# Performance work log

Hardware: AMD Instinct MI355X
Metric: run time of the kernel (lower is better)

Reference implementation:

```python
import jax, jax.numpy as jnp
import numpy as np
from jax.scipy.special import logsumexp

B, D, H, L, R, K = 4096, 784, 16, 4, 4, 8
D1 = D // 2
NBIS, NNEWT = 50, 3
LOG2PI = float(np.log(2.0 * np.pi))


def square_swish(h):
    # util.square_swish nonlinearity (swish-family; see notes)
    return h * jax.nn.sigmoid(h)


def mixture_terms(xv, logits, mu, log_s):
    # xv: [B, D1]; logits/mu/log_s: [B, D1, K]
    logw = jax.nn.log_softmax(logits, axis=-1)
    t = (xv[..., None] - mu) * jnp.exp(-log_s)
    log_cdf = logsumexp(logw + jax.nn.log_sigmoid(t), axis=-1)          # log F(x)
    log_sf = logsumexp(logw + jax.nn.log_sigmoid(-t), axis=-1)          # log (1-F(x))
    log_pdf = logsumexp(logw + jax.nn.log_sigmoid(t) + jax.nn.log_sigmoid(-t) - log_s, axis=-1)  # log F'(x)
    return log_cdf, log_sf, log_pdf


def invert_mixture_logit(y, logits, mu, log_s):
    # Solve logit(F(x)) = y for x: bisection (stop-grad) + Newton polish (differentiable).
    sl, sm, ss, sy = map(jax.lax.stop_gradient, (logits, mu, log_s, y))

    def body(_, lo_hi):
        lo, hi = lo_hi
        mid = 0.5 * (lo + hi)
        lc, lsf, _ = mixture_terms(mid, sl, sm, ss)
        f = lc - lsf - sy
        return jnp.where(f < 0, mid, lo), jnp.where(f < 0, hi, mid)

    lo = jnp.full_like(y, -100.0)
    hi = jnp.full_like(y, 100.0)
    lo, hi = jax.lax.fori_loop(0, NBIS, body, (lo, hi))
    xv = jax.lax.stop_gradient(0.5 * (lo + hi))
    for _ in range(NNEWT):
        lc, lsf, lp = mixture_terms(xv, logits, mu, log_s)
        logdet = lp - lc - lsf  # d/dx logit(F(x))
        xv = xv - (lc - lsf - y) * jnp.exp(-logdet)
    lc, lsf, lp = mixture_terms(xv, logits, mu, log_s)
    return xv, lp - lc - lsf


def conditioner(h_in, Wi, bi, W1l, b1l, W2l, b2l, Wo, bo):
    h = square_swish(h_in @ Wi + bi)
    for r in range(R):  # 4 resnet blocks, hidden_dim=16
        h = h + square_swish(h @ W1l[r] + b1l[r]) @ W2l[r] + b2l[r]
    return (h @ Wo + bo).reshape(-1, D1, 3 * K)


def flow_inverse(x, eps, W_in, b_in, W1, b1, W2, b2, W_out, b_out):
    # UnitGaussianPrior sample eps -> inverse coupling stack; log q via change of variables
    log_q = -0.5 * jnp.sum(eps * eps + LOG2PI, axis=-1)
    z = eps
    for l in reversed(range(L)):
        za, zb = z[:, :D1], z[:, D1:]
        if l % 2 == 1:
            za, zb = zb, za
        p = conditioner(jnp.concatenate([zb, x], axis=-1),
                        W_in[l], b_in[l], W1[l], b1[l], W2[l], b2[l], W_out[l], b_out[l])
        logits, mu, log_s = p[..., :K], p[..., K:2 * K], p[..., 2 * K:]
        xa, ld = invert_mixture_logit(za, logits, mu, log_s)
        log_q = log_q + jnp.sum(ld, axis=-1)
        if l % 2 == 0:
            z = jnp.concatenate([xa, zb], axis=-1)
        else:
            z = jnp.concatenate([zb, xa], axis=-1)
    return z, log_q


def setup_inputs():
    key = jax.random.key(0)
    ks = jax.random.split(key, 6)
    s_in = 1.0 / np.sqrt(D1 + D)
    s_h = 1.0 / np.sqrt(H)
    return {
        "x": jax.random.normal(ks[0], (B, D), jnp.float32),
        "eps": jax.random.normal(ks[1], (B, D), jnp.float32),
        "W_in": jax.random.normal(ks[2], (L, D1 + D, H), jnp.float32) * s_in,
        "b_in": jnp.zeros((L, H), jnp.float32),
        "W1": jax.random.normal(ks[3], (L, R, H, H), jnp.float32) * s_h,
        "b1": jnp.zeros((L, R, H), jnp.float32),
        "W2": jax.random.normal(ks[4], (L, R, H, H), jnp.float32) * s_h,
        "b2": jnp.zeros((L, R, H), jnp.float32),
        "W_out": jax.random.normal(ks[5], (L, H, D1 * 3 * K), jnp.float32) * 0.05,
        "b_out": jnp.zeros((L, D1 * 3 * K), jnp.float32),
    }


def reference(x, eps, W_in, b_in, W1, b1, W2, b2, W_out, b_out):
    return flow_inverse(x, eps, W_in, b_in, W1, b1, W2, b2, W_out, b_out)
```

## Files before the change

### kernel.cpp

```cpp
#include <hip/hip_runtime.h>
#include <math.h>

constexpr int cB   = 4096;
constexpr int cD   = 784;
constexpr int cD1  = 392;
constexpr int cH   = 16;
constexpr int cL   = 4;
constexpr int cR   = 4;
constexpr int cDIN = 1176;
constexpr int cPDIM = cD1 * 3 * 8;
#define LOG2PI_F 1.8378770664093453f
#define L2E_F    1.4426950408889634f
#define LN2_F    0.6931471805599453f
#define LN_LN2_F (-0.36651292058166432701f)

__device__ __forceinline__ float rcpf(float x)  { return __builtin_amdgcn_rcpf(x); }
__device__ __forceinline__ float exp2f_(float x){ return __builtin_amdgcn_exp2f(x); }
__device__ __forceinline__ float log2f_(float x){ return __builtin_amdgcn_logf(x); }
__device__ __forceinline__ float expn(float x)  { return exp2f_(x * L2E_F); }
__device__ __forceinline__ float logn(float x)  { return log2f_(x) * LN2_F; }

__global__ void __launch_bounds__(256) init_kernel(const float* __restrict__ eps,
                                                   float* __restrict__ logq) {
    const int wid  = threadIdx.x >> 6;
    const int lane = threadIdx.x & 63;
    const int b = blockIdx.x * 4 + wid;
    const float4* e = (const float4*)(eps + (size_t)b * cD);
    float sum = 0.f;
    for (int i = lane; i < cD / 4; i += 64) {
        float4 v = e[i];
        sum = fmaf(v.x, v.x, sum); sum = fmaf(v.y, v.y, sum);
        sum = fmaf(v.z, v.z, sum); sum = fmaf(v.w, v.w, sum);
    }
    #pragma unroll
    for (int off = 32; off; off >>= 1) sum += __shfl_xor(sum, off, 64);
    if (lane == 0) logq[b] = -0.5f * sum - 0.5f * (float)cD * LOG2PI_F;
}

__global__ void __launch_bounds__(256) mlp_kernel(
    const float* __restrict__ zbsrc, const float* __restrict__ x,
    const float* __restrict__ Win, const float* __restrict__ bin,
    const float* __restrict__ W1, const float* __restrict__ b1,
    const float* __restrict__ W2, const float* __restrict__ b2,
    float* __restrict__ hbuf)
{
    __shared__ float part[4][4][16];
    const int wid  = threadIdx.x >> 6;
    const int lane = threadIdx.x & 63;
    const int j = lane & 15;
    const int G = lane >> 4;
    const int bs = blockIdx.x * 8;
    const int sb = bs + (wid & 1) * 4;
    const int r0 = (wid >> 1) * 588;

    float acc[4][16];
    #pragma unroll
    for (int s = 0; s < 4; ++s)
        #pragma unroll
        for (int c = 0; c < 16; ++c) acc[s][c] = 0.f;

    const float* pz[4]; const float* px[4];
    #pragma unroll
    for (int s = 0; s < 4; ++s) {
        pz[s] = zbsrc + (size_t)(sb + s) * cD;
        px[s] = x + (size_t)(sb + s) * cD - cD1;
    }

    for (int i = r0 + lane; i < r0 + 588; i += 64) {
        const float4* wr = (const float4*)(Win + (size_t)i * cH);
        float4 w0 = wr[0], w1 = wr[1], w2 = wr[2], w3 = wr[3];
        float wv[16] = {w0.x,w0.y,w0.z,w0.w, w1.x,w1.y,w1.z,w1.w,
                        w2.x,w2.y,w2.z,w2.w, w3.x,w3.y,w3.z,w3.w};
        #pragma unroll
        for (int s = 0; s < 4; ++s) {
            const float* src = (i < cD1) ? pz[s] : px[s];
            float v = src[i];
            #pragma unroll
            for (int c = 0; c < 16; ++c) acc[s][c] = fmaf(v, wv[c], acc[s][c]);
        }
    }

    #pragma unroll
    for (int s = 0; s < 4; ++s) {
        #pragma unroll
        for (int c = 0; c < 8; ++c) {
            float sent = (lane & 8) ? acc[s][c] : acc[s][c + 8];
            float mine = (lane & 8) ? acc[s][c + 8] : acc[s][c];
            acc[s][c] = mine + __shfl_xor(sent, 8, 64);
        }
        #pragma unroll
        for (int c = 0; c < 4; ++c) {
            float sent = (lane & 4) ? acc[s][c] : acc[s][c + 4];
            float mine = (lane & 4) ? acc[s][c + 4] : acc[s][c];
            acc[s][c] = mine + __shfl_xor(sent, 4, 64);
        }
        #pragma unroll
        for (int c = 0; c < 2; ++c) {
            float sent = (lane & 2) ? acc[s][c] : acc[s][c + 2];
            float mine = (lane & 2) ? acc[s][c + 2] : acc[s][c];
            acc[s][c] = mine + __shfl_xor(sent, 2, 64);
        }
        {
            float sent = (lane & 1) ? acc[s][0] : acc[s][1];
            float mine = (lane & 1) ? acc[s][1] : acc[s][0];
            acc[s][0] = mine + __shfl_xor(sent, 1, 64);
        }
    }
    const int g4 = (lane >> 4) & 1, g5 = (lane >> 5) & 1;
    float a01, a23, colsum;
    {
        float sent = g4 ? acc[0][0] : acc[1][0];
        float keep = g4 ? acc[1][0] : acc[0][0];
        a01 = keep + __shfl_xor(sent, 16, 64);
    }
    {
        float sent = g4 ? acc[2][0] : acc[3][0];
        float keep = g4 ? acc[3][0] : acc[2][0];
        a23 = keep + __shfl_xor(sent, 16, 64);
    }
    {
        float sent = g5 ? a01 : a23;
        float keep = g5 ? a23 : a01;
        colsum = keep + __shfl_xor(sent, 32, 64);
    }

    part[wid][G][j] = colsum;
    __syncthreads();
    if (wid >= 2) return;

    colsum = part[wid][G][j] + part[wid + 2][G][j];

    float t0 = colsum + bin[j];
    float hj = t0 * rcpf(1.0f + expn(-t0));

    #pragma unroll
    for (int r = 0; r < cR; ++r) {
        const float* w1r = W1 + r * 256;
        const float* w2r = W2 + r * 256;
        float u = b1[r * 16 + j];
        #pragma unroll
        for (int i = 0; i < 16; ++i)
            u = fmaf(__shfl(hj, i, 16), w1r[i * 16 + j], u);
        u = u * rcpf(1.0f + expn(-u));
        float v = b2[r * 16 + j];
        #pragma unroll
        for (int i = 0; i < 16; ++i)
            v = fmaf(__shfl(u, i, 16), w2r[i * 16 + j], v);
        hj += v;
    }
    hbuf[(size_t)j * cB + (bs + wid * 4 + G)] = hj;
}

__global__ void __launch_bounds__(256) invert_kernel(
    float* __restrict__ z, const float* __restrict__ ysrc,
    const float* __restrict__ hbuf,
    const float* __restrict__ Wo, const float* __restrict__ bo,
    float* __restrict__ logq, int za_off)
{
    const int wid  = threadIdx.x >> 6;
    const int lane = threadIdx.x & 63;
    const int d = __builtin_amdgcn_readfirstlane(blockIdx.x * 4 + wid);
    const int b = blockIdx.y * 64 + lane;

    float hh[16];
    #pragma unroll
    for (int i = 0; i < 16; ++i) hh[i] = hbuf[(size_t)i * cB + b];

    float p[24];
    {
        const float4* bp = (const float4*)(bo + (size_t)d * 24);
        #pragma unroll
        for (int j4 = 0; j4 < 6; ++j4) {
            float4 v = bp[j4];
            p[j4*4+0] = v.x; p[j4*4+1] = v.y; p[j4*4+2] = v.z; p[j4*4+3] = v.w;
        }
        #pragma unroll
        for (int i = 0; i < 16; ++i) {
            float hv = hh[i];
            const float4* wr = (const float4*)(Wo + (size_t)i * cPDIM + (size_t)d * 24);
            #pragma unroll
            for (int j4 = 0; j4 < 6; ++j4) {
                float4 wv = wr[j4];
                p[j4*4+0] = fmaf(hv, wv.x, p[j4*4+0]);
                p[j4*4+1] = fmaf(hv, wv.y, p[j4*4+1]);
                p[j4*4+2] = fmaf(hv, wv.z, p[j4*4+2]);
                p[j4*4+3] = fmaf(hv, wv.w, p[j4*4+3]);
            }
        }
    }

    const float y0  = ysrc[(size_t)b * cD + za_off + d];
    const float sgn = (y0 < 0.f) ? -1.f : 1.f;
    const float yb  = fabsf(y0);

    float wt[8], pm[8], q2[8], is2[8], nm2[8], wis2[8];
    float S, lgSn, SLN2, lo, hi, x0;
    {
        float m = p[0];
        #pragma unroll
        for (int k = 1; k < 8; ++k) m = fmaxf(m, p[k]);
        S = 0.f;
        #pragma unroll
        for (int k = 0; k < 8; ++k) {
            pm[k] = p[k] - m;
            wt[k] = exp2f_(pm[k] * L2E_F);
            S += wt[k];
        }
        lgSn = log2f_(S) * LN2_F;
        SLN2 = S * LN2_F;
        float lo0 = 1e30f, hi0 = -1e30f, xa = 0.f;
        #pragma unroll
        for (int k = 0; k < 8; ++k) {
            q2[k] = p[16 + k] * L2E_F;
            float sk  = exp2f_(q2[k]);
            float ik  = exp2f_(-q2[k]);
            is2[k] = ik * L2E_F;
            float mub = sgn * p[8 + k];
            nm2[k] = -mub * is2[k];
            wis2[k] = wt[k] * is2[k];
            float inv = fmaf(yb, sk, mub);
            lo0 = fminf(lo0, inv); hi0 = fmaxf(hi0, inv);
            xa = fmaf(wt[k], inv, xa);
        }
        float pad = 1e-3f + 1e-5f * (fabsf(lo0) + fabsf(hi0));
        lo = lo0 - pad; hi = hi0 + pad;
        x0 = xa * rcpf(S);
    }

    float xv, ld;
    if (yb <= 30.0f) {
        xv = x0;
        #pragma unroll 1
        for (int it = 0; it < 3; ++it) {
            float sfv = 0.f, pdfa = 0.f;
            #pragma unroll
            for (int k = 0; k < 8; ++k) {
                float t2 = fmaf(xv, is2[k], nm2[k]);
                float e  = exp2f_(t2);
                float r  = rcpf(1.0f + e);
                sfv  = fmaf(wt[k], r, sfv);
                pdfa = fmaf(wis2[k], fmaf(-r, r, r), pdfa);
            }
            float cdf = S - sfv;
            float f = (log2f_(cdf) - log2f_(sfv)) * LN2_F;
            if (f < yb) lo = xv; else hi = xv;
            float step = (f - yb) * cdf * sfv * rcpf(pdfa * SLN2);
            float xn = xv - step;
            if (!(xn > lo && xn < hi)) xn = 0.5f * (lo + hi);
            xv = xn;
        }
        {
            float sfv = 0.f, pdfa = 0.f;
            #pragma unroll
            for (int k = 0; k < 8; ++k) {
                float t2 = fmaf(xv, is2[k], nm2[k]);
                float e  = exp2f_(t2);
                float r  = rcpf(1.0f + e);
                sfv  = fmaf(wt[k], r, sfv);
                pdfa = fmaf(wis2[k], fmaf(-r, r, r), pdfa);
            }
            float cdf = S - sfv;
            float l2c = log2f_(cdf), l2s = log2f_(sfv), l2p = log2f_(pdfa);
            ld = (l2p - l2c - l2s) * LN2_F + LN_LN2_F + lgSn;
            float f = (l2c - l2s) * LN2_F;
            if (f < yb) lo = xv; else hi = xv;
            float step = (f - yb) * cdf * sfv * rcpf(pdfa * SLN2);
            float xn = xv - step;
            if (!(xn > lo && xn < hi)) xn = 0.5f * (lo + hi);
            xv = xn;
        }
    } else {
        float lw[8], lis[8];
        #pragma unroll
        for (int k = 0; k < 8; ++k) {
            lw[k]  = pm[k] - lgSn;
            lis[k] = -q2[k] * LN2_F;
        }
        xv = x0;
        #pragma unroll 1
        for (int it = 0; it < 4; ++it) {
            float u[8];
            float mu_ = -1e30f;
            #pragma unroll
            for (int k = 0; k < 8; ++k) {
                float t  = fmaf(xv, is2[k], nm2[k]) * LN2_F;
                float ec = fminf(expn(-t), 1.0f);
                u[k] = lw[k] - t - ec * fmaf(-0.5f, ec, 1.0f);
                mu_ = fmaxf(mu_, u[k]);
            }
            float Su = 0.f;
            #pragma unroll
            for (int k = 0; k < 8; ++k) Su += expn(u[k] - mu_);
            float lsf = mu_ + logn(Su);
            float m2 = -1e30f;
            #pragma unroll
            for (int k = 0; k < 8; ++k) m2 = fmaxf(m2, u[k] + lis[k]);
            float S2 = 0.f;
            #pragma unroll
            for (int k = 0; k < 8; ++k) S2 += expn(u[k] + lis[k] - m2);
            float lp = m2 + logn(S2);
            if (it == 3) { ld = lp - lsf; break; }
            float f = -lsf;
            if (f < yb) lo = xv; else hi = xv;
            float step = (f - yb) * expn(lsf - lp);
            float xn = xv - step;
            if (!(xn > lo && xn < hi)) xn = 0.5f * (lo + hi);
            xv = xn;
        }
    }

    z[(size_t)b * cD + za_off + d] = sgn * xv;

    __shared__ float red[256];
    red[threadIdx.x] = ld;
    __syncthreads();
    if (wid == 0) {
        float ssum = red[lane] + red[lane + 64] + red[lane + 128] + red[lane + 192];
        atomicAdd(&logq[b], ssum);
    }
}

extern "C" void kernel_launch(void* const* d_in, const int* in_sizes, int n_in,
                              void* d_out, int out_size, void* d_ws, size_t ws_size,
                              hipStream_t stream) {
    const float* x     = (const float*)d_in[0];
    const float* eps   = (const float*)d_in[1];
    const float* W_in  = (const float*)d_in[2];
    const float* b_in  = (const float*)d_in[3];
    const float* W1    = (const float*)d_in[4];
    const float* b1    = (const float*)d_in[5];
    const float* W2    = (const float*)d_in[6];
    const float* b2    = (const float*)d_in[7];
    const float* W_out = (const float*)d_in[8];
    const float* b_out = (const float*)d_in[9];

    float* z    = (float*)d_out;
    float* logq = z + (size_t)cB * cD;
    float* hbuf = (float*)d_ws;

    init_kernel<<<cB / 4, 256, 0, stream>>>(eps, logq);

    for (int l = cL - 1; l >= 0; --l) {
        const int zb_off = (l & 1) ? 0 : cD1;
        const int za_off = (l & 1) ? cD1 : 0;
        const float* zbsrc = (l == 3) ? (eps + zb_off) : (z + zb_off);
        const float* ysrc  = (l >= 2) ? eps : z;
        mlp_kernel<<<cB / 8, 256, 0, stream>>>(
            zbsrc, x,
            W_in + (size_t)l * cDIN * cH, b_in + (size_t)l * cH,
            W1 + (size_t)l * cR * cH * cH, b1 + (size_t)l * cR * cH,
            W2 + (size_t)l * cR * cH * cH, b2 + (size_t)l * cR * cH,
            hbuf);
        invert_kernel<<<dim3(cD1 / 4, cB / 64), 256, 0, stream>>>(
            z, ysrc, hbuf,
            W_out + (size_t)l * cH * cPDIM, b_out + (size_t)l * cPDIM,
            logq, za_off);
    }
}
```

Before: 280.5 us.

## Precompute x-projection for all layers upfront and cut Newton iterations to two

The x part of the conditioner's input projection does not depend on the flow state, so it is computed once for all four layers in a fused precompute kernel alongside the log-prior, and each per-layer MLP kernel now only projects the 392 zb features. Separately, the safeguarded Newton loop in the inversion kernel drops from three iterations to two. This removes repeated reads of x and Win rows from the serial layer chain, at the cost of a workspace buffer. Fewer Newton iterations may reduce accuracy of the inverse relative to the reference.

```diff
diff --git a/kernel.cpp b/kernel.cpp
--- a/kernel.cpp
+++ b/kernel.cpp
@@ -20,25 +20,102 @@
 __device__ __forceinline__ float expn(float x)  { return exp2f_(x * L2E_F); }
 __device__ __forceinline__ float logn(float x)  { return log2f_(x) * LN2_F; }
 
-__global__ void __launch_bounds__(256) init_kernel(const float* __restrict__ eps,
-                                                   float* __restrict__ logq) {
+__device__ __forceinline__ float transpose_route(float acc[4][16], int lane) {
+    #pragma unroll
+    for (int s = 0; s < 4; ++s) {
+        #pragma unroll
+        for (int c = 0; c < 8; ++c) {
+            float sent = (lane & 8) ? acc[s][c] : acc[s][c + 8];
+            float mine = (lane & 8) ? acc[s][c + 8] : acc[s][c];
+            acc[s][c] = mine + __shfl_xor(sent, 8, 64);
+        }
+        #pragma unroll
+        for (int c = 0; c < 4; ++c) {
+            float sent = (lane & 4) ? acc[s][c] : acc[s][c + 4];
+            float mine = (lane & 4) ? acc[s][c + 4] : acc[s][c];
+            acc[s][c] = mine + __shfl_xor(sent, 4, 64);
+        }
+        #pragma unroll
+        for (int c = 0; c < 2; ++c) {
+            float sent = (lane & 2) ? acc[s][c] : acc[s][c + 2];
+            float mine = (lane & 2) ? acc[s][c + 2] : acc[s][c];
+            acc[s][c] = mine + __shfl_xor(sent, 2, 64);
+        }
+        {
+            float sent = (lane & 1) ? acc[s][0] : acc[s][1];
+            float mine = (lane & 1) ? acc[s][1] : acc[s][0];
+            acc[s][0] = mine + __shfl_xor(sent, 1, 64);
+        }
+    }
+    const int g4 = (lane >> 4) & 1, g5 = (lane >> 5) & 1;
+    float a01, a23;
+    {
+        float sent = g4 ? acc[0][0] : acc[1][0];
+        float keep = g4 ? acc[1][0] : acc[0][0];
+        a01 = keep + __shfl_xor(sent, 16, 64);
+    }
+    {
+        float sent = g4 ? acc[2][0] : acc[3][0];
+        float keep = g4 ? acc[3][0] : acc[2][0];
+        a23 = keep + __shfl_xor(sent, 16, 64);
+    }
+    float sent = g5 ? a01 : a23;
+    float keep = g5 ? a23 : a01;
+    return keep + __shfl_xor(sent, 32, 64);
+}
+
+__global__ void __launch_bounds__(256) precompute_kernel(
+    const float* __restrict__ eps, const float* __restrict__ x,
+    const float* __restrict__ Win_all,
+    float* __restrict__ logq, float* __restrict__ part_x)
+{
     const int wid  = threadIdx.x >> 6;
     const int lane = threadIdx.x & 63;
-    const int b = blockIdx.x * 4 + wid;
-    const float4* e = (const float4*)(eps + (size_t)b * cD);
-    float sum = 0.f;
-    for (int i = lane; i < cD / 4; i += 64) {
-        float4 v = e[i];
-        sum = fmaf(v.x, v.x, sum); sum = fmaf(v.y, v.y, sum);
-        sum = fmaf(v.z, v.z, sum); sum = fmaf(v.w, v.w, sum);
-    }
-    #pragma unroll
-    for (int off = 32; off; off >>= 1) sum += __shfl_xor(sum, off, 64);
-    if (lane == 0) logq[b] = -0.5f * sum - 0.5f * (float)cD * LOG2PI_F;
+    const int j = lane & 15;
+    const int G = lane >> 4;
+    const int bs = blockIdx.x * 4;
+
+    {
+        const float4* e = (const float4*)(eps + (size_t)(bs + wid) * cD);
+        float sum = 0.f;
+        for (int i = lane; i < cD / 4; i += 64) {
+            float4 v = e[i];
+            sum = fmaf(v.x, v.x, sum); sum = fmaf(v.y, v.y, sum);
+            sum = fmaf(v.z, v.z, sum); sum = fmaf(v.w, v.w, sum);
+        }
+        #pragma unroll
+        for (int off = 32; off; off >>= 1) sum += __shfl_xor(sum, off, 64);
+        if (lane == 0) logq[bs + wid] = -0.5f * sum - 0.5f * (float)cD * LOG2PI_F;
+    }
+
+    const float* W = Win_all + (size_t)wid * cDIN * cH + (size_t)cD1 * cH;
+    float acc[4][16];
+    #pragma unroll
+    for (int s = 0; s < 4; ++s)
+        #pragma unroll
+        for (int c = 0; c < 16; ++c) acc[s][c] = 0.f;
+    const float* px[4];
+    #pragma unroll
+    for (int s = 0; s < 4; ++s) px[s] = x + (size_t)(bs + s) * cD;
+
+    for (int i = lane; i < cD; i += 64) {
+        const float4* wr = (const float4*)(W + (size_t)i * cH);
+        float4 w0 = wr[0], w1 = wr[1], w2 = wr[2], w3 = wr[3];
+        float wv[16] = {w0.x,w0.y,w0.z,w0.w, w1.x,w1.y,w1.z,w1.w,
+                        w2.x,w2.y,w2.z,w2.w, w3.x,w3.y,w3.z,w3.w};
+        #pragma unroll
+        for (int s = 0; s < 4; ++s) {
+            float v = px[s][i];
+            #pragma unroll
+            for (int c = 0; c < 16; ++c) acc[s][c] = fmaf(v, wv[c], acc[s][c]);
+        }
+    }
+    float colsum = transpose_route(acc, lane);
+    part_x[((size_t)wid * cH + j) * cB + (bs + G)] = colsum;
 }
 
 __global__ void __launch_bounds__(256) mlp_kernel(
-    const float* __restrict__ zbsrc, const float* __restrict__ x,
+    const float* __restrict__ zbsrc, const float* __restrict__ pxl,
     const float* __restrict__ Win, const float* __restrict__ bin,
     const float* __restrict__ W1, const float* __restrict__ b1,
     const float* __restrict__ W2, const float* __restrict__ b2,
@@ -51,7 +128,7 @@
     const int G = lane >> 4;
     const int bs = blockIdx.x * 8;
     const int sb = bs + (wid & 1) * 4;
-    const int r0 = (wid >> 1) * 588;
+    const int r0 = (wid >> 1) * 196;
 
     float acc[4][16];
     #pragma unroll
@@ -59,76 +136,31 @@
         #pragma unroll
         for (int c = 0; c < 16; ++c) acc[s][c] = 0.f;
 
-    const float* pz[4]; const float* px[4];
-    #pragma unroll
-    for (int s = 0; s < 4; ++s) {
-        pz[s] = zbsrc + (size_t)(sb + s) * cD;
-        px[s] = x + (size_t)(sb + s) * cD - cD1;
-    }
-
-    for (int i = r0 + lane; i < r0 + 588; i += 64) {
+    const float* pz[4];
+    #pragma unroll
+    for (int s = 0; s < 4; ++s) pz[s] = zbsrc + (size_t)(sb + s) * cD;
+
+    for (int i = r0 + lane; i < r0 + 196; i += 64) {
         const float4* wr = (const float4*)(Win + (size_t)i * cH);
         float4 w0 = wr[0], w1 = wr[1], w2 = wr[2], w3 = wr[3];
         float wv[16] = {w0.x,w0.y,w0.z,w0.w, w1.x,w1.y,w1.z,w1.w,
                         w2.x,w2.y,w2.z,w2.w, w3.x,w3.y,w3.z,w3.w};
         #pragma unroll
         for (int s = 0; s < 4; ++s) {
-            const float* src = (i < cD1) ? pz[s] : px[s];
-            float v = src[i];
+            float v = pz[s][i];
             #pragma unroll
             for (int c = 0; c < 16; ++c) acc[s][c] = fmaf(v, wv[c], acc[s][c]);
         }
     }
 
-    #pragma unroll
-    for (int s = 0; s < 4; ++s) {
-        #pragma unroll
-        for (int c = 0; c < 8; ++c) {
-            float sent = (lane & 8) ? acc[s][c] : acc[s][c + 8];
-            float mine = (lane & 8) ? acc[s][c + 8] : acc[s][c];
-            acc[s][c] = mine + __shfl_xor(sent, 8, 64);
-        }
-        #pragma unroll
-        for (int c = 0; c < 4; ++c) {
-            float sent = (lane & 4) ? acc[s][c] : acc[s][c + 4];
-            float mine = (lane & 4) ? acc[s][c + 4] : acc[s][c];
-            acc[s][c] = mine + __shfl_xor(sent, 4, 64);
-        }
-        #pragma unroll
-        for (int c = 0; c < 2; ++c) {
-            float sent = (lane & 2) ? acc[s][c] : acc[s][c + 2];
-            float mine = (lane & 2) ? acc[s][c + 2] : acc[s][c];
-            acc[s][c] = mine + __shfl_xor(sent, 2, 64);
-        }
-        {
-            float sent = (lane & 1) ? acc[s][0] : acc[s][1];
-            float mine = (lane & 1) ? acc[s][1] : acc[s][0];
-            acc[s][0] = mine + __shfl_xor(sent, 1, 64);
-        }
-    }
-    const int g4 = (lane >> 4) & 1, g5 = (lane >> 5) & 1;
-    float a01, a23, colsum;
-    {
-        float sent = g4 ? acc[0][0] : acc[1][0];
-        float keep = g4 ? acc[1][0] : acc[0][0];
-        a01 = keep + __shfl_xor(sent, 16, 64);
-    }
-    {
-        float sent = g4 ? acc[2][0] : acc[3][0];
-        float keep = g4 ? acc[3][0] : acc[2][0];
-        a23 = keep + __shfl_xor(sent, 16, 64);
-    }
-    {
-        float sent = g5 ? a01 : a23;
-        float keep = g5 ? a23 : a01;
-        colsum = keep + __shfl_xor(sent, 32, 64);
-    }
-
+    float colsum = transpose_route(acc, lane);
     part[wid][G][j] = colsum;
     __syncthreads();
     if (wid >= 2) return;
 
-    colsum = part[wid][G][j] + part[wid + 2][G][j];
+    const int smp = bs + wid * 4 + G;
+    colsum = part[wid][G][j] + part[wid + 2][G][j]
+           + pxl[(size_t)j * cB + smp];
 
     float t0 = colsum + bin[j];
     float hj = t0 * rcpf(1.0f + expn(-t0));
@@ -148,7 +180,7 @@
             v = fmaf(__shfl(u, i, 16), w2r[i * 16 + j], v);
         hj += v;
     }
-    hbuf[(size_t)j * cB + (bs + wid * 4 + G)] = hj;
+    hbuf[(size_t)j * cB + smp] = hj;
 }
 
 __global__ void __launch_bounds__(256) invert_kernel(
@@ -231,7 +263,7 @@
     if (yb <= 30.0f) {
         xv = x0;
         #pragma unroll 1
-        for (int it = 0; it < 3; ++it) {
+        for (int it = 0; it < 2; ++it) {
             float sfv = 0.f, pdfa = 0.f;
             #pragma unroll
             for (int k = 0; k < 8; ++k) {
@@ -334,11 +366,12 @@
     const float* W_out = (const float*)d_in[8];
     const float* b_out = (const float*)d_in[9];
 
-    float* z    = (float*)d_out;
-    float* logq = z + (size_t)cB * cD;
-    float* hbuf = (float*)d_ws;
-
-    init_kernel<<<cB / 4, 256, 0, stream>>>(eps, logq);
+    float* z     = (float*)d_out;
+    float* logq  = z + (size_t)cB * cD;
+    float* hbuf  = (float*)d_ws;
+    float* partx = hbuf + (size_t)cH * cB;
+
+    precompute_kernel<<<cB / 4, 256, 0, stream>>>(eps, x, W_in, logq, partx);
 
     for (int l = cL - 1; l >= 0; --l) {
         const int zb_off = (l & 1) ? 0 : cD1;
@@ -346,7 +379,7 @@
         const float* zbsrc = (l == 3) ? (eps + zb_off) : (z + zb_off);
         const float* ysrc  = (l >= 2) ? eps : z;
         mlp_kernel<<<cB / 8, 256, 0, stream>>>(
-            zbsrc, x,
+            zbsrc, partx + (size_t)l * cH * cB,
             W_in + (size_t)l * cDIN * cH, b_in + (size_t)l * cH,
             W1 + (size_t)l * cR * cH * cH, b1 + (size_t)l * cR * cH,
             W2 + (size_t)l * cR * cH * cH, b2 + (size_t)l * cR * cH,
```

New measurement: 284.0 us. About the same (+1.3%).
